# Kernel optimization log

Hardware: AMD Instinct MI355X
Metric: run time of the kernel (lower is better)

The kernel has to match this reference:

```python
import jax, jax.numpy as jnp
import numpy as np
from jax import lax

H = 64          # GRU hidden size
OUT_STEPS = 20  # output_seq_size


def _maxpool2(x):
    # x: [N, C, H, W] -> 2x2 max pool, stride 2, VALID
    return lax.reduce_window(x, -jnp.inf, lax.max, (1, 1, 2, 2), (1, 1, 2, 2), 'VALID')


def _conv(x, w, b):
    # NCHW / OIHW, VALID, stride 1
    y = lax.conv_general_dilated(x, w, (1, 1), 'VALID',
                                 dimension_numbers=('NCHW', 'OIHW', 'NCHW'))
    return y + b[None, :, None, None]


def _gru_step(h, x, wih, whh, bih, bhh):
    # PyTorch GRU gate order: r, z, n
    gi = x @ wih.T + bih            # [B, 3H]
    gh = h @ whh.T + bhh            # [B, 3H]
    i_r, i_z, i_n = jnp.split(gi, 3, axis=-1)
    h_r, h_z, h_n = jnp.split(gh, 3, axis=-1)
    r = jax.nn.sigmoid(i_r + h_r)
    z = jax.nn.sigmoid(i_z + h_z)
    n = jnp.tanh(i_n + r * h_n)
    return (1.0 - z) * n + z * h


def setup_inputs() -> dict:
    key = jax.random.key(0)
    ks = jax.random.split(key, 20)
    B, T = 1024, 31
    s = 0.1
    return {
        'bbox_seq': jax.random.normal(ks[0], (B, T, 4), jnp.float32),
        'head_seq': jax.random.uniform(ks[1], (B, T, 32, 32), jnp.float32),
        'conv1_w': jax.random.normal(ks[2], (4, 1, 3, 3), jnp.float32) * s,
        'conv1_b': jax.random.normal(ks[3], (4,), jnp.float32) * s,
        'conv2_w': jax.random.normal(ks[4], (10, 4, 3, 3), jnp.float32) * s,
        'conv2_b': jax.random.normal(ks[5], (10,), jnp.float32) * s,
        'fc_w': jax.random.normal(ks[6], (5, 360), jnp.float32) * s,
        'fc_b': jax.random.normal(ks[7], (5,), jnp.float32) * s,
        'enc_wih': jax.random.normal(ks[8], (3 * H, 9), jnp.float32) * s,
        'enc_whh': jax.random.normal(ks[9], (3 * H, H), jnp.float32) * s,
        'enc_bih': jax.random.normal(ks[10], (3 * H,), jnp.float32) * s,
        'enc_bhh': jax.random.normal(ks[11], (3 * H,), jnp.float32) * s,
        'dec_wih': jax.random.normal(ks[12], (3 * H, 4), jnp.float32) * s,
        'dec_whh': jax.random.normal(ks[13], (3 * H, H), jnp.float32) * s,
        'dec_bih': jax.random.normal(ks[14], (3 * H,), jnp.float32) * s,
        'dec_bhh': jax.random.normal(ks[15], (3 * H,), jnp.float32) * s,
        'lin_w': jax.random.normal(ks[16], (4, H), jnp.float32) * s,
        'lin_b': jax.random.normal(ks[17], (4,), jnp.float32) * s,
    }


def reference(bbox_seq, head_seq, conv1_w, conv1_b, conv2_w, conv2_b, fc_w, fc_b,
              enc_wih, enc_whh, enc_bih, enc_bhh,
              dec_wih, dec_whh, dec_bih, dec_bhh, lin_w, lin_b):
    B, T = bbox_seq.shape[0], bbox_seq.shape[1]
    L = T - 1  # encoder sequence length

    # offset: last bbox, broadcast over OUT_STEPS -> [B, OUT_STEPS, 4]
    offset = jnp.broadcast_to(bbox_seq[:, -1][:, None, :], (B, OUT_STEPS, 4))

    diffs = bbox_seq[:, 1:] - bbox_seq[:, :-1]  # [B, L, 4] (dropout p=0 -> identity)

    # --- ConvEncoder on all head crops at once ---
    imgs = head_seq[:, :-1].reshape(B * L, 1, 32, 32)
    x = jax.nn.relu(_conv(imgs, conv1_w, conv1_b))   # [BL, 4, 30, 30]
    x = _maxpool2(x)                                  # [BL, 4, 15, 15]
    x = jax.nn.relu(_conv(x, conv2_w, conv2_b))       # [BL, 10, 13, 13]
    x = _maxpool2(x)                                  # [BL, 10, 6, 6]
    emb = x.reshape(B * L, -1) @ fc_w.T + fc_b        # [BL, 5]
    emb = emb.reshape(B, L, -1)

    enc_in = jnp.concatenate([diffs, emb], axis=2)    # [B, L, 9]

    # --- GRU encoder (scan over time) ---
    def enc_step(h, x_t):
        h = _gru_step(h, x_t, enc_wih, enc_whh, enc_bih, enc_bhh)
        return h, None
    h0 = jnp.zeros((B, H), enc_in.dtype)
    hn, _ = lax.scan(enc_step, h0, jnp.swapaxes(enc_in, 0, 1))

    def dec_step(carry, _):
        h, prev_x = carry
        h = _gru_step(h, prev_x, dec_wih, dec_whh, dec_bih, dec_bhh)
        x_new = h @ lin_w.T + lin_b + prev_x
        return (h, x_new), x_new
    (_, _), outs = lax.scan(dec_step, (hn, diffs[:, -1]), None, length=OUT_STEPS)
    out = jnp.swapaxes(outs, 0, 1)                    # [B, OUT_STEPS, 4]

    return jnp.cumsum(out, axis=1) + offset
```

## Files before the change

### kernel.cpp

```cpp
#include <hip/hip_runtime.h>
#include <hip/hip_bf16.h>


#define B_    1024
#define L_    30
#define H_    64

__device__ __forceinline__ float sigmoid_f(float v) {
    return 1.f / (1.f + __expf(-v));
}
__device__ __forceinline__ float tanh_f(float v) {
    v = fminf(fmaxf(v, -15.f), 15.f);
    float e = __expf(2.f * v);
    return (e - 1.f) / (e + 1.f);
}
__device__ __forceinline__ void load4_lds(float* r, const float* p) {
    float2 a = *(const float2*)p;
    float2 b = *(const float2*)(p + 2);
    r[0] = a.x; r[1] = a.y; r[2] = b.x; r[3] = b.y;
}

__global__ __launch_bounds__(64) void conv_embed_kernel(
    const float* __restrict__ bbox,
    const float* __restrict__ head,
    const float* __restrict__ c1w, const float* __restrict__ c1b,
    const float* __restrict__ c2w, const float* __restrict__ c2b,
    const float* __restrict__ fcw, const float* __restrict__ fcb,
    float* __restrict__ enc_in)
{
    const int img = blockIdx.x;
    const int b = img / L_;
    const int l = img % L_;
    const int tid = threadIdx.x;

    __shared__ float s_img[32 * 32];
    __shared__ float s_p1[4 * 15 * 16];
    __shared__ float s_p2[360];
    __shared__ float s_red[60];

    {
        const float4* src = (const float4*)(head + ((size_t)b * 31 + (size_t)l) * 1024);
        float4* dst = (float4*)s_img;
        #pragma unroll
        for (int i = 0; i < 4; ++i) dst[tid + 64 * i] = src[tid + 64 * i];
    }
    __syncthreads();

    if (tid < 60) {
        const int c = tid / 15, px = tid % 15;
        const int x0 = 2 * px;
        float w[9];
        #pragma unroll
        for (int k = 0; k < 9; ++k) w[k] = c1w[c * 9 + k];
        const float bias = c1b[c];

        float r0[4], r1[4], r2[4], r3[4];
        load4_lds(r0, s_img + 0 * 32 + x0);
        load4_lds(r1, s_img + 1 * 32 + x0);
        #pragma unroll
        for (int py = 0; py < 15; ++py) {
            load4_lds(r2, s_img + (2 * py + 2) * 32 + x0);
            load4_lds(r3, s_img + (2 * py + 3) * 32 + x0);
            float a00 = bias, a01 = bias, a10 = bias, a11 = bias;
            #pragma unroll
            for (int kx = 0; kx < 3; ++kx) {
                const float w0 = w[kx], w1 = w[3 + kx], w2 = w[6 + kx];
                a00 = fmaf(w0, r0[kx],     fmaf(w1, r1[kx],     fmaf(w2, r2[kx],     a00)));
                a01 = fmaf(w0, r0[kx + 1], fmaf(w1, r1[kx + 1], fmaf(w2, r2[kx + 1], a01)));
                a10 = fmaf(w0, r1[kx],     fmaf(w1, r2[kx],     fmaf(w2, r3[kx],     a10)));
                a11 = fmaf(w0, r1[kx + 1], fmaf(w1, r2[kx + 1], fmaf(w2, r3[kx + 1], a11)));
            }
            a00 = fmaxf(a00, 0.f); a01 = fmaxf(a01, 0.f);
            a10 = fmaxf(a10, 0.f); a11 = fmaxf(a11, 0.f);
            s_p1[c * 240 + py * 16 + px] = fmaxf(fmaxf(a00, a01), fmaxf(a10, a11));
            #pragma unroll
            for (int q = 0; q < 4; ++q) { r0[q] = r2[q]; r1[q] = r3[q]; }
        }
    }
    __syncthreads();

    if (tid < 60) {
        const int c = tid / 6, px = tid % 6;
        const int x0 = 2 * px;
        float w[4][9];
        #pragma unroll
        for (int ic = 0; ic < 4; ++ic)
            #pragma unroll
            for (int k = 0; k < 9; ++k) w[ic][k] = c2w[(c * 4 + ic) * 9 + k];
        const float bias = c2b[c];

        float win[4][4][4];
        #pragma unroll
        for (int ic = 0; ic < 4; ++ic) {
            load4_lds(win[0][ic], s_p1 + ic * 240 + 0 * 16 + x0);
            load4_lds(win[1][ic], s_p1 + ic * 240 + 1 * 16 + x0);
        }
        #pragma unroll
        for (int py = 0; py < 6; ++py) {
            #pragma unroll
            for (int ic = 0; ic < 4; ++ic) {
                load4_lds(win[2][ic], s_p1 + ic * 240 + (2 * py + 2) * 16 + x0);
                load4_lds(win[3][ic], s_p1 + ic * 240 + (2 * py + 3) * 16 + x0);
            }
            float a00 = bias, a01 = bias, a10 = bias, a11 = bias;
            #pragma unroll
            for (int ic = 0; ic < 4; ++ic) {
                #pragma unroll
                for (int kx = 0; kx < 3; ++kx) {
                    const float w0 = w[ic][kx], w1 = w[ic][3 + kx], w2 = w[ic][6 + kx];
                    a00 = fmaf(w0, win[0][ic][kx],     fmaf(w1, win[1][ic][kx],     fmaf(w2, win[2][ic][kx],     a00)));
                    a01 = fmaf(w0, win[0][ic][kx + 1], fmaf(w1, win[1][ic][kx + 1], fmaf(w2, win[2][ic][kx + 1], a01)));
                    a10 = fmaf(w0, win[1][ic][kx],     fmaf(w1, win[2][ic][kx],     fmaf(w2, win[3][ic][kx],     a10)));
                    a11 = fmaf(w0, win[1][ic][kx + 1], fmaf(w1, win[2][ic][kx + 1], fmaf(w2, win[3][ic][kx + 1], a11)));
                }
            }
            a00 = fmaxf(a00, 0.f); a01 = fmaxf(a01, 0.f);
            a10 = fmaxf(a10, 0.f); a11 = fmaxf(a11, 0.f);
            s_p2[c * 36 + py * 6 + px] = fmaxf(fmaxf(a00, a01), fmaxf(a10, a11));
            #pragma unroll
            for (int ic = 0; ic < 4; ++ic)
                #pragma unroll
                for (int q = 0; q < 4; ++q) { win[0][ic][q] = win[2][ic][q]; win[1][ic][q] = win[3][ic][q]; }
        }
    }
    __syncthreads();

    if (tid < 60) {
        const int o = tid / 12, i0 = tid % 12;
        const float* wrow = fcw + o * 360;
        float acc = 0.f;
        #pragma unroll
        for (int k = 0; k < 30; ++k) {
            const int i = i0 + 12 * k;
            acc = fmaf(wrow[i], s_p2[i], acc);
        }
        s_red[tid] = acc;
    }
    __syncthreads();

    float* dst = enc_in + ((size_t)b * L_ + l) * 9;
    if (tid < 5) {
        float acc = fcb[tid];
        #pragma unroll
        for (int k = 0; k < 12; ++k) acc += s_red[tid * 12 + k];
        dst[4 + tid] = acc;
    } else if (tid >= 8 && tid < 12) {
        const int d = tid - 8;
        const float* bb = bbox + (size_t)b * 124 + (size_t)l * 4;
        dst[d] = bb[4 + d] - bb[d];
    }
}

__global__ __launch_bounds__(256) void gru_enc_kernel(
    const float* __restrict__ enc_in,
    const float* __restrict__ wih,
    const float* __restrict__ whh,
    const float* __restrict__ bih,
    const float* __restrict__ bhh,
    float* __restrict__ hn)
{
    const int b = blockIdx.x;
    const int tid = threadIdx.x;
    const int w = tid >> 6, j = tid & 63;

    float Wh[3][16];
    #pragma unroll
    for (int g = 0; g < 3; ++g) {
        const float* row = whh + (g * 64 + j) * 64 + w * 16;
        #pragma unroll
        for (int k = 0; k < 16; ++k) Wh[g][k] = row[k];
    }
    float Wi[3][9];
    #pragma unroll
    for (int g = 0; g < 3; ++g) {
        const float* row = wih + (g * 64 + j) * 9;
        #pragma unroll
        for (int k = 0; k < 9; ++k) Wi[g][k] = row[k];
    }
    const float bi0 = bih[j], bi1 = bih[64 + j], bi2 = bih[128 + j];
    const float bh0 = bhh[j], bh1 = bhh[64 + j], bh2 = bhh[128 + j];

    __shared__ float sp[2][4][3][64];
    float h = 0.f;
    const float* xp = enc_in + (size_t)b * (L_ * 9);

    for (int t = 0; t < L_; ++t) {
        const int pb = t & 1;
        float pr = 0.f, pz = 0.f, pn = 0.f;
        #pragma unroll
        for (int k = 0; k < 16; ++k) {
            const float hk = __shfl(h, w * 16 + k);
            pr = fmaf(Wh[0][k], hk, pr);
            pz = fmaf(Wh[1][k], hk, pz);
            pn = fmaf(Wh[2][k], hk, pn);
        }
        sp[pb][w][0][j] = pr;
        sp[pb][w][1][j] = pz;
        sp[pb][w][2][j] = pn;

        float x[9];
        #pragma unroll
        for (int k = 0; k < 9; ++k) x[k] = xp[t * 9 + k];
        float gr = bi0 + bh0, gz = bi1 + bh1, gni = bi2, gnh = bh2;
        #pragma unroll
        for (int k = 0; k < 9; ++k) {
            gr  = fmaf(Wi[0][k], x[k], gr);
            gz  = fmaf(Wi[1][k], x[k], gz);
            gni = fmaf(Wi[2][k], x[k], gni);
        }
        __syncthreads();
        #pragma unroll
        for (int ww = 0; ww < 4; ++ww) {
            gr  += sp[pb][ww][0][j];
            gz  += sp[pb][ww][1][j];
            gnh += sp[pb][ww][2][j];
        }
        const float r = sigmoid_f(gr);
        const float z = sigmoid_f(gz);
        const float n = tanh_f(gni + r * gnh);
        h = (1.f - z) * n + z * h;
    }
    if (w == 0) hn[(size_t)b * H_ + j] = h;
}

__global__ __launch_bounds__(256) void gru_dec_kernel(
    const float* __restrict__ bbox,
    const float* __restrict__ hn,
    const float* __restrict__ wih,
    const float* __restrict__ whh,
    const float* __restrict__ bih,
    const float* __restrict__ bhh,
    const float* __restrict__ linw,
    const float* __restrict__ linb,
    float* __restrict__ out)
{
    const int b = blockIdx.x;
    const int tid = threadIdx.x;
    const int w = tid >> 6, j = tid & 63;

    float Wh[3][16];
    #pragma unroll
    for (int g = 0; g < 3; ++g) {
        const float* row = whh + (g * 64 + j) * 64 + w * 16;
        #pragma unroll
        for (int k = 0; k < 16; ++k) Wh[g][k] = row[k];
    }
    float Wi[3][4];
    #pragma unroll
    for (int g = 0; g < 3; ++g) {
        const float* row = wih + (g * 64 + j) * 4;
        #pragma unroll
        for (int k = 0; k < 4; ++k) Wi[g][k] = row[k];
    }
    const float bi0 = bih[j], bi1 = bih[64 + j], bi2 = bih[128 + j];
    const float bh0 = bhh[j], bh1 = bhh[64 + j], bh2 = bhh[128 + j];
    const float lw0 = linw[j], lw1 = linw[64 + j], lw2 = linw[128 + j], lw3 = linw[192 + j];
    const float lb0 = linb[0], lb1 = linb[1], lb2 = linb[2], lb3 = linb[3];

    float h = hn[(size_t)b * H_ + j];
    const float* bb = bbox + (size_t)b * 124;
    float px0 = bb[120] - bb[116];
    float px1 = bb[121] - bb[117];
    float px2 = bb[122] - bb[118];
    float px3 = bb[123] - bb[119];
    const float of0 = bb[120], of1 = bb[121], of2 = bb[122], of3 = bb[123];
    float cs0 = 0.f, cs1 = 0.f, cs2 = 0.f, cs3 = 0.f;

    __shared__ float sp[2][4][3][64];
    float* outp = out + (size_t)b * 80;

    for (int t = 0; t < 20; ++t) {
        const int pb = t & 1;
        float pr = 0.f, pz = 0.f, pn = 0.f;
        #pragma unroll
        for (int k = 0; k < 16; ++k) {
            const float hk = __shfl(h, w * 16 + k);
            pr = fmaf(Wh[0][k], hk, pr);
            pz = fmaf(Wh[1][k], hk, pz);
            pn = fmaf(Wh[2][k], hk, pn);
        }
        sp[pb][w][0][j] = pr;
        sp[pb][w][1][j] = pz;
        sp[pb][w][2][j] = pn;

        float gr = bi0 + bh0, gz = bi1 + bh1, gni = bi2, gnh = bh2;
        gr  = fmaf(Wi[0][0], px0, fmaf(Wi[0][1], px1, fmaf(Wi[0][2], px2, fmaf(Wi[0][3], px3, gr))));
        gz  = fmaf(Wi[1][0], px0, fmaf(Wi[1][1], px1, fmaf(Wi[1][2], px2, fmaf(Wi[1][3], px3, gz))));
        gni = fmaf(Wi[2][0], px0, fmaf(Wi[2][1], px1, fmaf(Wi[2][2], px2, fmaf(Wi[2][3], px3, gni))));

        __syncthreads();
        #pragma unroll
        for (int ww = 0; ww < 4; ++ww) {
            gr  += sp[pb][ww][0][j];
            gz  += sp[pb][ww][1][j];
            gnh += sp[pb][ww][2][j];
        }
        const float r = sigmoid_f(gr);
        const float z = sigmoid_f(gz);
        const float n = tanh_f(gni + r * gnh);
        h = (1.f - z) * n + z * h;

        float v0 = lw0 * h, v1 = lw1 * h, v2 = lw2 * h, v3 = lw3 * h;
        #pragma unroll
        for (int s = 32; s > 0; s >>= 1) {
            v0 += __shfl_xor(v0, s);
            v1 += __shfl_xor(v1, s);
            v2 += __shfl_xor(v2, s);
            v3 += __shfl_xor(v3, s);
        }
        px0 = v0 + lb0 + px0;
        px1 = v1 + lb1 + px1;
        px2 = v2 + lb2 + px2;
        px3 = v3 + lb3 + px3;
        cs0 += px0; cs1 += px1; cs2 += px2; cs3 += px3;
        if (tid == 0) {
            outp[t * 4 + 0] = cs0 + of0;
            outp[t * 4 + 1] = cs1 + of1;
            outp[t * 4 + 2] = cs2 + of2;
            outp[t * 4 + 3] = cs3 + of3;
        }
    }
}

extern "C" void kernel_launch(void* const* d_in, const int* in_sizes, int n_in,
                              void* d_out, int out_size, void* d_ws, size_t ws_size,
                              hipStream_t stream) {
    (void)in_sizes; (void)n_in; (void)out_size; (void)ws_size;
    const float* bbox = (const float*)d_in[0];
    const float* head = (const float*)d_in[1];
    const float* c1w  = (const float*)d_in[2];
    const float* c1b  = (const float*)d_in[3];
    const float* c2w  = (const float*)d_in[4];
    const float* c2b  = (const float*)d_in[5];
    const float* fcw  = (const float*)d_in[6];
    const float* fcb  = (const float*)d_in[7];
    const float* ewih = (const float*)d_in[8];
    const float* ewhh = (const float*)d_in[9];
    const float* ebih = (const float*)d_in[10];
    const float* ebhh = (const float*)d_in[11];
    const float* dwih = (const float*)d_in[12];
    const float* dwhh = (const float*)d_in[13];
    const float* dbih = (const float*)d_in[14];
    const float* dbhh = (const float*)d_in[15];
    const float* linw = (const float*)d_in[16];
    const float* linb = (const float*)d_in[17];
    float* out = (float*)d_out;

    float* enc_in = (float*)d_ws;
    float* hn     = enc_in + (size_t)B_ * L_ * 9;

    conv_embed_kernel<<<B_ * L_, 64, 0, stream>>>(bbox, head, c1w, c1b, c2w, c2b,
                                                  fcw, fcb, enc_in);
    gru_enc_kernel<<<B_, 256, 0, stream>>>(enc_in, ewih, ewhh, ebih, ebhh, hn);
    gru_dec_kernel<<<B_, 256, 0, stream>>>(bbox, hn, dwih, dwhh, dbih, dbhh,
                                           linw, linb, out);
}
```

Baseline: 341.4 us.

## Split GRU recurrences across two waves with readlane broadcast and prefetched inputs

The encoder and decoder GRU kernels now use 128 threads per sequence, two waves each covering 32 hidden inputs, where before four waves covered 16 each. The hidden-state broadcast uses readlane with compile-time lanes in place of shfl, and the cross-wave reduction reads only the partner wave's partial sums from LDS. The next step's encoder input is prefetched during the current step, weights are loaded with float4, and the decoder writes its output as one float4. The aim is less LDS reduction and sync cost per step, in exchange for longer per-thread FMA chains and more weight registers.

```diff
diff --git a/kernel.cpp b/kernel.cpp
--- a/kernel.cpp
+++ b/kernel.cpp
@@ -13,6 +13,9 @@
     v = fminf(fmaxf(v, -15.f), 15.f);
     float e = __expf(2.f * v);
     return (e - 1.f) / (e + 1.f);
+}
+__device__ __forceinline__ float bcast(float v, int lane) {
+    return __int_as_float(__builtin_amdgcn_readlane(__float_as_int(v), lane));
 }
 __device__ __forceinline__ void load4_lds(float* r, const float* p) {
     float2 a = *(const float2*)p;
@@ -151,7 +154,7 @@
     }
 }
 
-__global__ __launch_bounds__(256) void gru_enc_kernel(
+__global__ __launch_bounds__(128) void gru_enc_kernel(
     const float* __restrict__ enc_in,
     const float* __restrict__ wih,
     const float* __restrict__ whh,
@@ -159,16 +162,16 @@
     const float* __restrict__ bhh,
     float* __restrict__ hn)
 {
-    const int b = blockIdx.x;
-    const int tid = threadIdx.x;
-    const int w = tid >> 6, j = tid & 63;
-
-    float Wh[3][16];
+    const int j  = threadIdx.x & 63;
+    const int w2 = threadIdx.x >> 6;
+    const int b  = blockIdx.x;
+
+    float Wh[3][32];
     #pragma unroll
     for (int g = 0; g < 3; ++g) {
-        const float* row = whh + (g * 64 + j) * 64 + w * 16;
-        #pragma unroll
-        for (int k = 0; k < 16; ++k) Wh[g][k] = row[k];
+        const float4* row = (const float4*)(whh + (size_t)(g * 64 + j) * 64 + 32 * w2);
+        #pragma unroll
+        for (int k4 = 0; k4 < 8; ++k4) *(float4*)&Wh[g][4 * k4] = row[k4];
     }
     float Wi[3][9];
     #pragma unroll
@@ -180,50 +183,65 @@
     const float bi0 = bih[j], bi1 = bih[64 + j], bi2 = bih[128 + j];
     const float bh0 = bhh[j], bh1 = bhh[64 + j], bh2 = bhh[128 + j];
 
-    __shared__ float sp[2][4][3][64];
+    __shared__ float sp[2][2][3][64];
     float h = 0.f;
     const float* xp = enc_in + (size_t)b * (L_ * 9);
 
+    float xr[9];
+    #pragma unroll
+    for (int k = 0; k < 9; ++k) xr[k] = xp[k];
+
     for (int t = 0; t < L_; ++t) {
         const int pb = t & 1;
+
         float pr = 0.f, pz = 0.f, pn = 0.f;
-        #pragma unroll
-        for (int k = 0; k < 16; ++k) {
-            const float hk = __shfl(h, w * 16 + k);
-            pr = fmaf(Wh[0][k], hk, pr);
-            pz = fmaf(Wh[1][k], hk, pz);
-            pn = fmaf(Wh[2][k], hk, pn);
-        }
-        sp[pb][w][0][j] = pr;
-        sp[pb][w][1][j] = pz;
-        sp[pb][w][2][j] = pn;
-
-        float x[9];
-        #pragma unroll
-        for (int k = 0; k < 9; ++k) x[k] = xp[t * 9 + k];
-        float gr = bi0 + bh0, gz = bi1 + bh1, gni = bi2, gnh = bh2;
+        if (w2 == 0) {
+            #pragma unroll
+            for (int k = 0; k < 32; ++k) {
+                const float hk = bcast(h, k);
+                pr = fmaf(Wh[0][k], hk, pr);
+                pz = fmaf(Wh[1][k], hk, pz);
+                pn = fmaf(Wh[2][k], hk, pn);
+            }
+        } else {
+            #pragma unroll
+            for (int k = 0; k < 32; ++k) {
+                const float hk = bcast(h, k + 32);
+                pr = fmaf(Wh[0][k], hk, pr);
+                pz = fmaf(Wh[1][k], hk, pz);
+                pn = fmaf(Wh[2][k], hk, pn);
+            }
+        }
+        sp[pb][w2][0][j] = pr;
+        sp[pb][w2][1][j] = pz;
+        sp[pb][w2][2][j] = pn;
+
+        float gr = bi0 + bh0, gz = bi1 + bh1, gni = bi2;
         #pragma unroll
         for (int k = 0; k < 9; ++k) {
-            gr  = fmaf(Wi[0][k], x[k], gr);
-            gz  = fmaf(Wi[1][k], x[k], gz);
-            gni = fmaf(Wi[2][k], x[k], gni);
-        }
+            gr  = fmaf(Wi[0][k], xr[k], gr);
+            gz  = fmaf(Wi[1][k], xr[k], gz);
+            gni = fmaf(Wi[2][k], xr[k], gni);
+        }
+        if (t + 1 < L_) {
+            #pragma unroll
+            for (int k = 0; k < 9; ++k) xr[k] = xp[(t + 1) * 9 + k];
+        }
+
         __syncthreads();
-        #pragma unroll
-        for (int ww = 0; ww < 4; ++ww) {
-            gr  += sp[pb][ww][0][j];
-            gz  += sp[pb][ww][1][j];
-            gnh += sp[pb][ww][2][j];
-        }
-        const float r = sigmoid_f(gr);
-        const float z = sigmoid_f(gz);
-        const float n = tanh_f(gni + r * gnh);
+        const float opr = sp[pb][w2 ^ 1][0][j];
+        const float opz = sp[pb][w2 ^ 1][1][j];
+        const float opn = sp[pb][w2 ^ 1][2][j];
+
+        const float r = sigmoid_f(gr + pr + opr);
+        const float z = sigmoid_f(gz + pz + opz);
+        const float n = tanh_f(gni + r * (bh2 + pn + opn));
         h = (1.f - z) * n + z * h;
     }
-    if (w == 0) hn[(size_t)b * H_ + j] = h;
-}
-
-__global__ __launch_bounds__(256) void gru_dec_kernel(
+    if (w2 == 0) hn[(size_t)b * H_ + j] = h;
+}
+
+__global__ __launch_bounds__(128) void gru_dec_kernel(
     const float* __restrict__ bbox,
     const float* __restrict__ hn,
     const float* __restrict__ wih,
@@ -234,16 +252,16 @@
     const float* __restrict__ linb,
     float* __restrict__ out)
 {
-    const int b = blockIdx.x;
-    const int tid = threadIdx.x;
-    const int w = tid >> 6, j = tid & 63;
-
-    float Wh[3][16];
+    const int j  = threadIdx.x & 63;
+    const int w2 = threadIdx.x >> 6;
+    const int b  = blockIdx.x;
+
+    float Wh[3][32];
     #pragma unroll
     for (int g = 0; g < 3; ++g) {
-        const float* row = whh + (g * 64 + j) * 64 + w * 16;
-        #pragma unroll
-        for (int k = 0; k < 16; ++k) Wh[g][k] = row[k];
+        const float4* row = (const float4*)(whh + (size_t)(g * 64 + j) * 64 + 32 * w2);
+        #pragma unroll
+        for (int k4 = 0; k4 < 8; ++k4) *(float4*)&Wh[g][4 * k4] = row[k4];
     }
     float Wi[3][4];
     #pragma unroll
@@ -266,38 +284,47 @@
     const float of0 = bb[120], of1 = bb[121], of2 = bb[122], of3 = bb[123];
     float cs0 = 0.f, cs1 = 0.f, cs2 = 0.f, cs3 = 0.f;
 
-    __shared__ float sp[2][4][3][64];
-    float* outp = out + (size_t)b * 80;
+    __shared__ float sp[2][2][3][64];
+    float4* outp = (float4*)(out + (size_t)b * 80);
 
     for (int t = 0; t < 20; ++t) {
         const int pb = t & 1;
+
         float pr = 0.f, pz = 0.f, pn = 0.f;
-        #pragma unroll
-        for (int k = 0; k < 16; ++k) {
-            const float hk = __shfl(h, w * 16 + k);
-            pr = fmaf(Wh[0][k], hk, pr);
-            pz = fmaf(Wh[1][k], hk, pz);
-            pn = fmaf(Wh[2][k], hk, pn);
-        }
-        sp[pb][w][0][j] = pr;
-        sp[pb][w][1][j] = pz;
-        sp[pb][w][2][j] = pn;
-
-        float gr = bi0 + bh0, gz = bi1 + bh1, gni = bi2, gnh = bh2;
+        if (w2 == 0) {
+            #pragma unroll
+            for (int k = 0; k < 32; ++k) {
+                const float hk = bcast(h, k);
+                pr = fmaf(Wh[0][k], hk, pr);
+                pz = fmaf(Wh[1][k], hk, pz);
+                pn = fmaf(Wh[2][k], hk, pn);
+            }
+        } else {
+            #pragma unroll
+            for (int k = 0; k < 32; ++k) {
+                const float hk = bcast(h, k + 32);
+                pr = fmaf(Wh[0][k], hk, pr);
+                pz = fmaf(Wh[1][k], hk, pz);
+                pn = fmaf(Wh[2][k], hk, pn);
+            }
+        }
+        sp[pb][w2][0][j] = pr;
+        sp[pb][w2][1][j] = pz;
+        sp[pb][w2][2][j] = pn;
+
+        float gr = bi0 + bh0, gz = bi1 + bh1, gni = bi2;
         gr  = fmaf(Wi[0][0], px0, fmaf(Wi[0][1], px1, fmaf(Wi[0][2], px2, fmaf(Wi[0][3], px3, gr))));
         gz  = fmaf(Wi[1][0], px0, fmaf(Wi[1][1], px1, fmaf(Wi[1][2], px2, fmaf(Wi[1][3], px3, gz))));
         gni = fmaf(Wi[2][0], px0, fmaf(Wi[2][1], px1, fmaf(Wi[2][2], px2, fmaf(Wi[2][3], px3, gni))));
 
         __syncthreads();
-        #pragma unroll
-        for (int ww = 0; ww < 4; ++ww) {
-            gr  += sp[pb][ww][0][j];
-            gz  += sp[pb][ww][1][j];
-            gnh += sp[pb][ww][2][j];
-        }
-        const float r = sigmoid_f(gr);
-        const float z = sigmoid_f(gz);
-        const float n = tanh_f(gni + r * gnh);
+        const float opr = sp[pb][w2 ^ 1][0][j];
+        const float opz = sp[pb][w2 ^ 1][1][j];
+        const float opn = sp[pb][w2 ^ 1][2][j];
+
+        const float r = sigmoid_f(gr + pr + opr);
+        const float z = sigmoid_f(gz + pz + opz);
+        const float n = tanh_f(gni + r * (bh2 + pn + opn));
         h = (1.f - z) * n + z * h;
 
         float v0 = lw0 * h, v1 = lw1 * h, v2 = lw2 * h, v3 = lw3 * h;
@@ -313,12 +340,7 @@
         px2 = v2 + lb2 + px2;
         px3 = v3 + lb3 + px3;
         cs0 += px0; cs1 += px1; cs2 += px2; cs3 += px3;
-        if (tid == 0) {
-            outp[t * 4 + 0] = cs0 + of0;
-            outp[t * 4 + 1] = cs1 + of1;
-            outp[t * 4 + 2] = cs2 + of2;
-            outp[t * 4 + 3] = cs3 + of3;
-        }
+        if (threadIdx.x == 0) outp[t] = make_float4(cs0 + of0, cs1 + of1, cs2 + of2, cs3 + of3);
     }
 }
 
@@ -351,7 +373,7 @@
 
     conv_embed_kernel<<<B_ * L_, 64, 0, stream>>>(bbox, head, c1w, c1b, c2w, c2b,
                                                   fcw, fcb, enc_in);
-    gru_enc_kernel<<<B_, 256, 0, stream>>>(enc_in, ewih, ewhh, ebih, ebhh, hn);
-    gru_dec_kernel<<<B_, 256, 0, stream>>>(bbox, hn, dwih, dwhh, dbih, dbhh,
+    gru_enc_kernel<<<B_, 128, 0, stream>>>(enc_in, ewih, ewhh, ebih, ebhh, hn);
+    gru_dec_kernel<<<B_, 128, 0, stream>>>(bbox, hn, dwih, dwhh, dbih, dbhh,
                                            linw, linb, out);
 }
```

New measurement: 322.4 us. -5.6%, faster.

## Fuse conv embedding, GRU encoder and decoder into a single kernel

Applied to the files above, without the earlier changes.

Merges the three kernels into one block-per-batch kernel: each wave computes conv embeddings for a subset of timesteps into shared memory, then the block runs the encoder and decoder GRUs. This removes the global enc_in/hn intermediates and two kernel launches. In exchange, the conv phase loses fine-grained parallelism and adds block-wide barriers, and the larger shared-memory footprint limits occupancy.

```diff
diff --git a/kernel.cpp b/kernel.cpp
--- a/kernel.cpp
+++ b/kernel.cpp
@@ -20,304 +20,282 @@
     r[0] = a.x; r[1] = a.y; r[2] = b.x; r[3] = b.y;
 }
 
-__global__ __launch_bounds__(64) void conv_embed_kernel(
+__global__ __launch_bounds__(256, 4) void fused_all_kernel(
     const float* __restrict__ bbox,
     const float* __restrict__ head,
     const float* __restrict__ c1w, const float* __restrict__ c1b,
     const float* __restrict__ c2w, const float* __restrict__ c2b,
     const float* __restrict__ fcw, const float* __restrict__ fcb,
-    float* __restrict__ enc_in)
-{
-    const int img = blockIdx.x;
-    const int b = img / L_;
-    const int l = img % L_;
-    const int tid = threadIdx.x;
-
-    __shared__ float s_img[32 * 32];
-    __shared__ float s_p1[4 * 15 * 16];
-    __shared__ float s_p2[360];
-    __shared__ float s_red[60];
-
-    {
-        const float4* src = (const float4*)(head + ((size_t)b * 31 + (size_t)l) * 1024);
-        float4* dst = (float4*)s_img;
-        #pragma unroll
-        for (int i = 0; i < 4; ++i) dst[tid + 64 * i] = src[tid + 64 * i];
-    }
-    __syncthreads();
-
-    if (tid < 60) {
-        const int c = tid / 15, px = tid % 15;
-        const int x0 = 2 * px;
-        float w[9];
-        #pragma unroll
-        for (int k = 0; k < 9; ++k) w[k] = c1w[c * 9 + k];
-        const float bias = c1b[c];
-
-        float r0[4], r1[4], r2[4], r3[4];
-        load4_lds(r0, s_img + 0 * 32 + x0);
-        load4_lds(r1, s_img + 1 * 32 + x0);
-        #pragma unroll
-        for (int py = 0; py < 15; ++py) {
-            load4_lds(r2, s_img + (2 * py + 2) * 32 + x0);
-            load4_lds(r3, s_img + (2 * py + 3) * 32 + x0);
-            float a00 = bias, a01 = bias, a10 = bias, a11 = bias;
-            #pragma unroll
-            for (int kx = 0; kx < 3; ++kx) {
-                const float w0 = w[kx], w1 = w[3 + kx], w2 = w[6 + kx];
-                a00 = fmaf(w0, r0[kx],     fmaf(w1, r1[kx],     fmaf(w2, r2[kx],     a00)));
-                a01 = fmaf(w0, r0[kx + 1], fmaf(w1, r1[kx + 1], fmaf(w2, r2[kx + 1], a01)));
-                a10 = fmaf(w0, r1[kx],     fmaf(w1, r2[kx],     fmaf(w2, r3[kx],     a10)));
-                a11 = fmaf(w0, r1[kx + 1], fmaf(w1, r2[kx + 1], fmaf(w2, r3[kx + 1], a11)));
-            }
-            a00 = fmaxf(a00, 0.f); a01 = fmaxf(a01, 0.f);
-            a10 = fmaxf(a10, 0.f); a11 = fmaxf(a11, 0.f);
-            s_p1[c * 240 + py * 16 + px] = fmaxf(fmaxf(a00, a01), fmaxf(a10, a11));
-            #pragma unroll
-            for (int q = 0; q < 4; ++q) { r0[q] = r2[q]; r1[q] = r3[q]; }
-        }
-    }
-    __syncthreads();
-
-    if (tid < 60) {
-        const int c = tid / 6, px = tid % 6;
-        const int x0 = 2 * px;
-        float w[4][9];
-        #pragma unroll
-        for (int ic = 0; ic < 4; ++ic)
-            #pragma unroll
-            for (int k = 0; k < 9; ++k) w[ic][k] = c2w[(c * 4 + ic) * 9 + k];
-        const float bias = c2b[c];
-
-        float win[4][4][4];
-        #pragma unroll
-        for (int ic = 0; ic < 4; ++ic) {
-            load4_lds(win[0][ic], s_p1 + ic * 240 + 0 * 16 + x0);
-            load4_lds(win[1][ic], s_p1 + ic * 240 + 1 * 16 + x0);
-        }
-        #pragma unroll
-        for (int py = 0; py < 6; ++py) {
-            #pragma unroll
-            for (int ic = 0; ic < 4; ++ic) {
-                load4_lds(win[2][ic], s_p1 + ic * 240 + (2 * py + 2) * 16 + x0);
-                load4_lds(win[3][ic], s_p1 + ic * 240 + (2 * py + 3) * 16 + x0);
-            }
-            float a00 = bias, a01 = bias, a10 = bias, a11 = bias;
-            #pragma unroll
-            for (int ic = 0; ic < 4; ++ic) {
-                #pragma unroll
-                for (int kx = 0; kx < 3; ++kx) {
-                    const float w0 = w[ic][kx], w1 = w[ic][3 + kx], w2 = w[ic][6 + kx];
-                    a00 = fmaf(w0, win[0][ic][kx],     fmaf(w1, win[1][ic][kx],     fmaf(w2, win[2][ic][kx],     a00)));
-                    a01 = fmaf(w0, win[0][ic][kx + 1], fmaf(w1, win[1][ic][kx + 1], fmaf(w2, win[2][ic][kx + 1], a01)));
-                    a10 = fmaf(w0, win[1][ic][kx],     fmaf(w1, win[2][ic][kx],     fmaf(w2, win[3][ic][kx],     a10)));
-                    a11 = fmaf(w0, win[1][ic][kx + 1], fmaf(w1, win[2][ic][kx + 1], fmaf(w2, win[3][ic][kx + 1], a11)));
-                }
-            }
-            a00 = fmaxf(a00, 0.f); a01 = fmaxf(a01, 0.f);
-            a10 = fmaxf(a10, 0.f); a11 = fmaxf(a11, 0.f);
-            s_p2[c * 36 + py * 6 + px] = fmaxf(fmaxf(a00, a01), fmaxf(a10, a11));
-            #pragma unroll
-            for (int ic = 0; ic < 4; ++ic)
-                #pragma unroll
-                for (int q = 0; q < 4; ++q) { win[0][ic][q] = win[2][ic][q]; win[1][ic][q] = win[3][ic][q]; }
-        }
-    }
-    __syncthreads();
-
-    if (tid < 60) {
-        const int o = tid / 12, i0 = tid % 12;
-        const float* wrow = fcw + o * 360;
-        float acc = 0.f;
-        #pragma unroll
-        for (int k = 0; k < 30; ++k) {
-            const int i = i0 + 12 * k;
-            acc = fmaf(wrow[i], s_p2[i], acc);
-        }
-        s_red[tid] = acc;
-    }
-    __syncthreads();
-
-    float* dst = enc_in + ((size_t)b * L_ + l) * 9;
-    if (tid < 5) {
-        float acc = fcb[tid];
-        #pragma unroll
-        for (int k = 0; k < 12; ++k) acc += s_red[tid * 12 + k];
-        dst[4 + tid] = acc;
-    } else if (tid >= 8 && tid < 12) {
-        const int d = tid - 8;
-        const float* bb = bbox + (size_t)b * 124 + (size_t)l * 4;
-        dst[d] = bb[4 + d] - bb[d];
-    }
-}
-
-__global__ __launch_bounds__(256) void gru_enc_kernel(
-    const float* __restrict__ enc_in,
-    const float* __restrict__ wih,
-    const float* __restrict__ whh,
-    const float* __restrict__ bih,
-    const float* __restrict__ bhh,
-    float* __restrict__ hn)
-{
-    const int b = blockIdx.x;
-    const int tid = threadIdx.x;
-    const int w = tid >> 6, j = tid & 63;
-
-    float Wh[3][16];
-    #pragma unroll
-    for (int g = 0; g < 3; ++g) {
-        const float* row = whh + (g * 64 + j) * 64 + w * 16;
-        #pragma unroll
-        for (int k = 0; k < 16; ++k) Wh[g][k] = row[k];
-    }
-    float Wi[3][9];
-    #pragma unroll
-    for (int g = 0; g < 3; ++g) {
-        const float* row = wih + (g * 64 + j) * 9;
-        #pragma unroll
-        for (int k = 0; k < 9; ++k) Wi[g][k] = row[k];
-    }
-    const float bi0 = bih[j], bi1 = bih[64 + j], bi2 = bih[128 + j];
-    const float bh0 = bhh[j], bh1 = bhh[64 + j], bh2 = bhh[128 + j];
-
-    __shared__ float sp[2][4][3][64];
-    float h = 0.f;
-    const float* xp = enc_in + (size_t)b * (L_ * 9);
-
-    for (int t = 0; t < L_; ++t) {
-        const int pb = t & 1;
-        float pr = 0.f, pz = 0.f, pn = 0.f;
-        #pragma unroll
-        for (int k = 0; k < 16; ++k) {
-            const float hk = __shfl(h, w * 16 + k);
-            pr = fmaf(Wh[0][k], hk, pr);
-            pz = fmaf(Wh[1][k], hk, pz);
-            pn = fmaf(Wh[2][k], hk, pn);
-        }
-        sp[pb][w][0][j] = pr;
-        sp[pb][w][1][j] = pz;
-        sp[pb][w][2][j] = pn;
-
-        float x[9];
-        #pragma unroll
-        for (int k = 0; k < 9; ++k) x[k] = xp[t * 9 + k];
-        float gr = bi0 + bh0, gz = bi1 + bh1, gni = bi2, gnh = bh2;
-        #pragma unroll
-        for (int k = 0; k < 9; ++k) {
-            gr  = fmaf(Wi[0][k], x[k], gr);
-            gz  = fmaf(Wi[1][k], x[k], gz);
-            gni = fmaf(Wi[2][k], x[k], gni);
-        }
-        __syncthreads();
-        #pragma unroll
-        for (int ww = 0; ww < 4; ++ww) {
-            gr  += sp[pb][ww][0][j];
-            gz  += sp[pb][ww][1][j];
-            gnh += sp[pb][ww][2][j];
-        }
-        const float r = sigmoid_f(gr);
-        const float z = sigmoid_f(gz);
-        const float n = tanh_f(gni + r * gnh);
-        h = (1.f - z) * n + z * h;
-    }
-    if (w == 0) hn[(size_t)b * H_ + j] = h;
-}
-
-__global__ __launch_bounds__(256) void gru_dec_kernel(
-    const float* __restrict__ bbox,
-    const float* __restrict__ hn,
-    const float* __restrict__ wih,
-    const float* __restrict__ whh,
-    const float* __restrict__ bih,
-    const float* __restrict__ bhh,
-    const float* __restrict__ linw,
-    const float* __restrict__ linb,
+    const float* __restrict__ ewih, const float* __restrict__ ewhh,
+    const float* __restrict__ ebih, const float* __restrict__ ebhh,
+    const float* __restrict__ dwih, const float* __restrict__ dwhh,
+    const float* __restrict__ dbih, const float* __restrict__ dbhh,
+    const float* __restrict__ linw, const float* __restrict__ linb,
     float* __restrict__ out)
 {
     const int b = blockIdx.x;
     const int tid = threadIdx.x;
-    const int w = tid >> 6, j = tid & 63;
-
-    float Wh[3][16];
-    #pragma unroll
-    for (int g = 0; g < 3; ++g) {
-        const float* row = whh + (g * 64 + j) * 64 + w * 16;
+    const int w = tid >> 6, lane = tid & 63;
+
+    __shared__ float smem[9904];
+    float* enc_s = smem + 9632;
+    float* wb    = smem + w * 2408;
+    float* s_img = wb;
+    float* s_p1  = wb + 1024;
+    float* s_p2  = wb + 1984;
+    float* s_red = wb + 2344;
+    float* sp    = smem;
+
+    for (int it = 0; it < 8; ++it) {
+        const int l = it * 4 + w;
+        const bool act = (l < L_);
+
+        if (act) {
+            const float4* src = (const float4*)(head + ((size_t)b * 31 + (size_t)l) * 1024);
+            float4* dst = (float4*)s_img;
+            #pragma unroll
+            for (int i = 0; i < 4; ++i) dst[lane + 64 * i] = src[lane + 64 * i];
+        }
+        __syncthreads();
+
+        if (act && lane < 60) {
+            const int c = lane / 15, px = lane % 15;
+            const int x0 = 2 * px;
+            float wg[9];
+            #pragma unroll
+            for (int k = 0; k < 9; ++k) wg[k] = c1w[c * 9 + k];
+            const float bias = c1b[c];
+
+            float r0[4], r1[4], r2[4], r3[4];
+            load4_lds(r0, s_img + 0 * 32 + x0);
+            load4_lds(r1, s_img + 1 * 32 + x0);
+            #pragma unroll
+            for (int py = 0; py < 15; ++py) {
+                load4_lds(r2, s_img + (2 * py + 2) * 32 + x0);
+                load4_lds(r3, s_img + (2 * py + 3) * 32 + x0);
+                float a00 = bias, a01 = bias, a10 = bias, a11 = bias;
+                #pragma unroll
+                for (int kx = 0; kx < 3; ++kx) {
+                    const float w0 = wg[kx], w1 = wg[3 + kx], w2 = wg[6 + kx];
+                    a00 = fmaf(w0, r0[kx],     fmaf(w1, r1[kx],     fmaf(w2, r2[kx],     a00)));
+                    a01 = fmaf(w0, r0[kx + 1], fmaf(w1, r1[kx + 1], fmaf(w2, r2[kx + 1], a01)));
+                    a10 = fmaf(w0, r1[kx],     fmaf(w1, r2[kx],     fmaf(w2, r3[kx],     a10)));
+                    a11 = fmaf(w0, r1[kx + 1], fmaf(w1, r2[kx + 1], fmaf(w2, r3[kx + 1], a11)));
+                }
+                a00 = fmaxf(a00, 0.f); a01 = fmaxf(a01, 0.f);
+                a10 = fmaxf(a10, 0.f); a11 = fmaxf(a11, 0.f);
+                s_p1[c * 240 + py * 16 + px] = fmaxf(fmaxf(a00, a01), fmaxf(a10, a11));
+                #pragma unroll
+                for (int q = 0; q < 4; ++q) { r0[q] = r2[q]; r1[q] = r3[q]; }
+            }
+        }
+        __syncthreads();
+
+        if (act && lane < 60) {
+            const int c = lane / 6, px = lane % 6;
+            const int x0 = 2 * px;
+            float wg[4][9];
+            #pragma unroll
+            for (int ic = 0; ic < 4; ++ic)
+                #pragma unroll
+                for (int k = 0; k < 9; ++k) wg[ic][k] = c2w[(c * 4 + ic) * 9 + k];
+            const float bias = c2b[c];
+
+            float win[4][4][4];
+            #pragma unroll
+            for (int ic = 0; ic < 4; ++ic) {
+                load4_lds(win[0][ic], s_p1 + ic * 240 + 0 * 16 + x0);
+                load4_lds(win[1][ic], s_p1 + ic * 240 + 1 * 16 + x0);
+            }
+            #pragma unroll
+            for (int py = 0; py < 6; ++py) {
+                #pragma unroll
+                for (int ic = 0; ic < 4; ++ic) {
+                    load4_lds(win[2][ic], s_p1 + ic * 240 + (2 * py + 2) * 16 + x0);
+                    load4_lds(win[3][ic], s_p1 + ic * 240 + (2 * py + 3) * 16 + x0);
+                }
+                float a00 = bias, a01 = bias, a10 = bias, a11 = bias;
+                #pragma unroll
+                for (int ic = 0; ic < 4; ++ic) {
+                    #pragma unroll
+                    for (int kx = 0; kx < 3; ++kx) {
+                        const float w0 = wg[ic][kx], w1 = wg[ic][3 + kx], w2 = wg[ic][6 + kx];
+                        a00 = fmaf(w0, win[0][ic][kx],     fmaf(w1, win[1][ic][kx],     fmaf(w2, win[2][ic][kx],     a00)));
+                        a01 = fmaf(w0, win[0][ic][kx + 1], fmaf(w1, win[1][ic][kx + 1], fmaf(w2, win[2][ic][kx + 1], a01)));
+                        a10 = fmaf(w0, win[1][ic][kx],     fmaf(w1, win[2][ic][kx],     fmaf(w2, win[3][ic][kx],     a10)));
+                        a11 = fmaf(w0, win[1][ic][kx + 1], fmaf(w1, win[2][ic][kx + 1], fmaf(w2, win[3][ic][kx + 1], a11)));
+                    }
+                }
+                a00 = fmaxf(a00, 0.f); a01 = fmaxf(a01, 0.f);
+                a10 = fmaxf(a10, 0.f); a11 = fmaxf(a11, 0.f);
+                s_p2[c * 36 + py * 6 + px] = fmaxf(fmaxf(a00, a01), fmaxf(a10, a11));
+                #pragma unroll
+                for (int ic = 0; ic < 4; ++ic)
+                    #pragma unroll
+                    for (int q = 0; q < 4; ++q) { win[0][ic][q] = win[2][ic][q]; win[1][ic][q] = win[3][ic][q]; }
+            }
+        }
+        __syncthreads();
+
+        if (act && lane < 60) {
+            const int o = lane / 12, i0 = lane % 12;
+            const float* wrow = fcw + o * 360;
+            float acc = 0.f;
+            #pragma unroll
+            for (int k = 0; k < 30; ++k) {
+                const int i = i0 + 12 * k;
+                acc = fmaf(wrow[i], s_p2[i], acc);
+            }
+            s_red[lane] = acc;
+        }
+        __syncthreads();
+
+        if (act) {
+            if (lane < 5) {
+                float acc = fcb[lane];
+                #pragma unroll
+                for (int k = 0; k < 12; ++k) acc += s_red[lane * 12 + k];
+                enc_s[l * 9 + 4 + lane] = acc;
+            } else if (lane >= 8 && lane < 12) {
+                const int d = lane - 8;
+                const float* bb = bbox + (size_t)b * 124 + (size_t)l * 4;
+                enc_s[l * 9 + d] = bb[4 + d] - bb[d];
+            }
+        }
+    }
+    __syncthreads();
+
+    const int j = lane;
+    float h = 0.f;
+
+    {
+        float Wh[3][16];
         #pragma unroll
-        for (int k = 0; k < 16; ++k) Wh[g][k] = row[k];
+        for (int g = 0; g < 3; ++g) {
+            const float4* row = (const float4*)(ewhh + (size_t)(g * 64 + j) * 64 + w * 16);
+            #pragma unroll
+            for (int k4 = 0; k4 < 4; ++k4) *(float4*)&Wh[g][4 * k4] = row[k4];
+        }
+        float Wi[3][9];
+        #pragma unroll
+        for (int g = 0; g < 3; ++g) {
+            const float* row = ewih + (g * 64 + j) * 9;
+            #pragma unroll
+            for (int k = 0; k < 9; ++k) Wi[g][k] = row[k];
+        }
+        const float bi0 = ebih[j], bi1 = ebih[64 + j], bi2 = ebih[128 + j];
+        const float bh0 = ebhh[j], bh1 = ebhh[64 + j], bh2 = ebhh[128 + j];
+
+        for (int t = 0; t < L_; ++t) {
+            const int pb = t & 1;
+            float pr = 0.f, pz = 0.f, pn = 0.f;
+            #pragma unroll
+            for (int k = 0; k < 16; ++k) {
+                const float hk = __shfl(h, w * 16 + k);
+                pr = fmaf(Wh[0][k], hk, pr);
+                pz = fmaf(Wh[1][k], hk, pz);
+                pn = fmaf(Wh[2][k], hk, pn);
+            }
+            sp[((pb * 4 + w) * 3 + 0) * 64 + j] = pr;
+            sp[((pb * 4 + w) * 3 + 1) * 64 + j] = pz;
+            sp[((pb * 4 + w) * 3 + 2) * 64 + j] = pn;
+
+            float gr = bi0 + bh0, gz = bi1 + bh1, gni = bi2, gnh = bh2;
+            #pragma unroll
+            for (int k = 0; k < 9; ++k) {
+                const float xk = enc_s[t * 9 + k];
+                gr  = fmaf(Wi[0][k], xk, gr);
+                gz  = fmaf(Wi[1][k], xk, gz);
+                gni = fmaf(Wi[2][k], xk, gni);
+            }
+            __syncthreads();
+            #pragma unroll
+            for (int ww = 0; ww < 4; ++ww) {
+                gr  += sp[((pb * 4 + ww) * 3 + 0) * 64 + j];
+                gz  += sp[((pb * 4 + ww) * 3 + 1) * 64 + j];
+                gnh += sp[((pb * 4 + ww) * 3 + 2) * 64 + j];
+            }
+            const float r = sigmoid_f(gr);
+            const float z = sigmoid_f(gz);
+            const float n = tanh_f(gni + r * gnh);
+            h = (1.f - z) * n + z * h;
+        }
     }
-    float Wi[3][4];
-    #pragma unroll
-    for (int g = 0; g < 3; ++g) {
-        const float* row = wih + (g * 64 + j) * 4;
+
+    {
+        float Wh[3][16];
         #pragma unroll
-        for (int k = 0; k < 4; ++k) Wi[g][k] = row[k];
-    }
-    const float bi0 = bih[j], bi1 = bih[64 + j], bi2 = bih[128 + j];
-    const float bh0 = bhh[j], bh1 = bhh[64 + j], bh2 = bhh[128 + j];
-    const float lw0 = linw[j], lw1 = linw[64 + j], lw2 = linw[128 + j], lw3 = linw[192 + j];
-    const float lb0 = linb[0], lb1 = linb[1], lb2 = linb[2], lb3 = linb[3];
-
-    float h = hn[(size_t)b * H_ + j];
-    const float* bb = bbox + (size_t)b * 124;
-    float px0 = bb[120] - bb[116];
-    float px1 = bb[121] - bb[117];
-    float px2 = bb[122] - bb[118];
-    float px3 = bb[123] - bb[119];
-    const float of0 = bb[120], of1 = bb[121], of2 = bb[122], of3 = bb[123];
-    float cs0 = 0.f, cs1 = 0.f, cs2 = 0.f, cs3 = 0.f;
-
-    __shared__ float sp[2][4][3][64];
-    float* outp = out + (size_t)b * 80;
-
-    for (int t = 0; t < 20; ++t) {
-        const int pb = t & 1;
-        float pr = 0.f, pz = 0.f, pn = 0.f;
+        for (int g = 0; g < 3; ++g) {
+            const float4* row = (const float4*)(dwhh + (size_t)(g * 64 + j) * 64 + w * 16);
+            #pragma unroll
+            for (int k4 = 0; k4 < 4; ++k4) *(float4*)&Wh[g][4 * k4] = row[k4];
+        }
+        float Wi[3][4];
         #pragma unroll
-        for (int k = 0; k < 16; ++k) {
-            const float hk = __shfl(h, w * 16 + k);
-            pr = fmaf(Wh[0][k], hk, pr);
-            pz = fmaf(Wh[1][k], hk, pz);
-            pn = fmaf(Wh[2][k], hk, pn);
-        }
-        sp[pb][w][0][j] = pr;
-        sp[pb][w][1][j] = pz;
-        sp[pb][w][2][j] = pn;
-
-        float gr = bi0 + bh0, gz = bi1 + bh1, gni = bi2, gnh = bh2;
-        gr  = fmaf(Wi[0][0], px0, fmaf(Wi[0][1], px1, fmaf(Wi[0][2], px2, fmaf(Wi[0][3], px3, gr))));
-        gz  = fmaf(Wi[1][0], px0, fmaf(Wi[1][1], px1, fmaf(Wi[1][2], px2, fmaf(Wi[1][3], px3, gz))));
-        gni = fmaf(Wi[2][0], px0, fmaf(Wi[2][1], px1, fmaf(Wi[2][2], px2, fmaf(Wi[2][3], px3, gni))));
-
-        __syncthreads();
-        #pragma unroll
-        for (int ww = 0; ww < 4; ++ww) {
-            gr  += sp[pb][ww][0][j];
-            gz  += sp[pb][ww][1][j];
-            gnh += sp[pb][ww][2][j];
-        }
-        const float r = sigmoid_f(gr);
-        const float z = sigmoid_f(gz);
-        const float n = tanh_f(gni + r * gnh);
-        h = (1.f - z) * n + z * h;
-
-        float v0 = lw0 * h, v1 = lw1 * h, v2 = lw2 * h, v3 = lw3 * h;
-        #pragma unroll
-        for (int s = 32; s > 0; s >>= 1) {
-            v0 += __shfl_xor(v0, s);
-            v1 += __shfl_xor(v1, s);
-            v2 += __shfl_xor(v2, s);
-            v3 += __shfl_xor(v3, s);
-        }
-        px0 = v0 + lb0 + px0;
-        px1 = v1 + lb1 + px1;
-        px2 = v2 + lb2 + px2;
-        px3 = v3 + lb3 + px3;
-        cs0 += px0; cs1 += px1; cs2 += px2; cs3 += px3;
-        if (tid == 0) {
-            outp[t * 4 + 0] = cs0 + of0;
-            outp[t * 4 + 1] = cs1 + of1;
-            outp[t * 4 + 2] = cs2 + of2;
-            outp[t * 4 + 3] = cs3 + of3;
+        for (int g = 0; g < 3; ++g) {
+            const float* row = dwih + (g * 64 + j) * 4;
+            #pragma unroll
+            for (int k = 0; k < 4; ++k) Wi[g][k] = row[k];
+        }
+        const float bi0 = dbih[j], bi1 = dbih[64 + j], bi2 = dbih[128 + j];
+        const float bh0 = dbhh[j], bh1 = dbhh[64 + j], bh2 = dbhh[128 + j];
+        const float lw0 = linw[j], lw1 = linw[64 + j], lw2 = linw[128 + j], lw3 = linw[192 + j];
+        const float lb0 = linb[0], lb1 = linb[1], lb2 = linb[2], lb3 = linb[3];
+
+        const float* bb = bbox + (size_t)b * 124;
+        float px0 = bb[120] - bb[116];
+        float px1 = bb[121] - bb[117];
+        float px2 = bb[122] - bb[118];
+        float px3 = bb[123] - bb[119];
+        const float of0 = bb[120], of1 = bb[121], of2 = bb[122], of3 = bb[123];
+        float cs0 = 0.f, cs1 = 0.f, cs2 = 0.f, cs3 = 0.f;
+        float4* outp = (float4*)(out + (size_t)b * 80);
+
+        for (int t = 0; t < 20; ++t) {
+            const int pb = t & 1;
+            float pr = 0.f, pz = 0.f, pn = 0.f;
+            #pragma unroll
+            for (int k = 0; k < 16; ++k) {
+                const float hk = __shfl(h, w * 16 + k);
+                pr = fmaf(Wh[0][k], hk, pr);
+                pz = fmaf(Wh[1][k], hk, pz);
+                pn = fmaf(Wh[2][k], hk, pn);
+            }
+            sp[((pb * 4 + w) * 3 + 0) * 64 + j] = pr;
+            sp[((pb * 4 + w) * 3 + 1) * 64 + j] = pz;
+            sp[((pb * 4 + w) * 3 + 2) * 64 + j] = pn;
+
+            float gr = bi0 + bh0, gz = bi1 + bh1, gni = bi2, gnh = bh2;
+            gr  = fmaf(Wi[0][0], px0, fmaf(Wi[0][1], px1, fmaf(Wi[0][2], px2, fmaf(Wi[0][3], px3, gr))));
+            gz  = fmaf(Wi[1][0], px0, fmaf(Wi[1][1], px1, fmaf(Wi[1][2], px2, fmaf(Wi[1][3], px3, gz))));
+            gni = fmaf(Wi[2][0], px0, fmaf(Wi[2][1], px1, fmaf(Wi[2][2], px2, fmaf(Wi[2][3], px3, gni))));
+
+            __syncthreads();
+            #pragma unroll
+            for (int ww = 0; ww < 4; ++ww) {
+                gr  += sp[((pb * 4 + ww) * 3 + 0) * 64 + j];
+                gz  += sp[((pb * 4 + ww) * 3 + 1) * 64 + j];
+                gnh += sp[((pb * 4 + ww) * 3 + 2) * 64 + j];
+            }
+            const float r = sigmoid_f(gr);
+            const float z = sigmoid_f(gz);
+            const float n = tanh_f(gni + r * gnh);
+            h = (1.f - z) * n + z * h;
+
+            float v0 = lw0 * h, v1 = lw1 * h, v2 = lw2 * h, v3 = lw3 * h;
+            #pragma unroll
+            for (int s = 32; s > 0; s >>= 1) {
+                v0 += __shfl_xor(v0, s);
+                v1 += __shfl_xor(v1, s);
+                v2 += __shfl_xor(v2, s);
+                v3 += __shfl_xor(v3, s);
+            }
+            px0 = v0 + lb0 + px0;
+            px1 = v1 + lb1 + px1;
+            px2 = v2 + lb2 + px2;
+            px3 = v3 + lb3 + px3;
+            cs0 += px0; cs1 += px1; cs2 += px2; cs3 += px3;
+            if (tid == 0) outp[t] = make_float4(cs0 + of0, cs1 + of1, cs2 + of2, cs3 + of3);
         }
     }
 }
@@ -325,7 +303,7 @@
 extern "C" void kernel_launch(void* const* d_in, const int* in_sizes, int n_in,
                               void* d_out, int out_size, void* d_ws, size_t ws_size,
                               hipStream_t stream) {
-    (void)in_sizes; (void)n_in; (void)out_size; (void)ws_size;
+    (void)in_sizes; (void)n_in; (void)out_size; (void)d_ws; (void)ws_size;
     const float* bbox = (const float*)d_in[0];
     const float* head = (const float*)d_in[1];
     const float* c1w  = (const float*)d_in[2];
@@ -346,12 +324,8 @@
     const float* linb = (const float*)d_in[17];
     float* out = (float*)d_out;
 
-    float* enc_in = (float*)d_ws;
-    float* hn     = enc_in + (size_t)B_ * L_ * 9;
-
-    conv_embed_kernel<<<B_ * L_, 64, 0, stream>>>(bbox, head, c1w, c1b, c2w, c2b,
-                                                  fcw, fcb, enc_in);
-    gru_enc_kernel<<<B_, 256, 0, stream>>>(enc_in, ewih, ewhh, ebih, ebhh, hn);
-    gru_dec_kernel<<<B_, 256, 0, stream>>>(bbox, hn, dwih, dwhh, dbih, dbhh,
-                                           linw, linb, out);
-}
+    fused_all_kernel<<<B_, 256, 0, stream>>>(bbox, head, c1w, c1b, c2w, c2b,
+                                             fcw, fcb, ewih, ewhh, ebih, ebhh,
+                                             dwih, dwhh, dbih, dbhh, linw, linb,
+                                             out);
+}
```

Result: slower. 360.4 us (+5.6%).
